# Kernel tuning notes

Hardware: AMD Instinct MI355X
Metric: run time of the kernel (lower is better)

The kernel has to match this reference:

```python
import jax, jax.numpy as jnp
import numpy as np
import math

VOCAB = 32000; D = 256; H = 8; HD = D // H; S = 2048; MLP = 1024; NC = 2
B = 4; L = 4; VEC = 8; M = S // VEC; MMA_K = 16; SPARSITY = 0.9


def _pos_encoding():
    pos = jnp.arange(S, dtype=jnp.float32)[:, None]
    div = jnp.exp(jnp.arange(0, D, 2, dtype=jnp.float32) * (-math.log(10000.0) / D))
    ang = pos * div  # [S, D//2]
    # interleave sin (even dims) / cos (odd dims)
    return jnp.stack([jnp.sin(ang), jnp.cos(ang)], axis=-1).reshape(S, D)


def _ln(x, g, b):
    mu = x.mean(-1, keepdims=True)
    var = x.var(-1, keepdims=True)
    return (x - mu) / jnp.sqrt(var + 1e-5) * g + b


def setup_inputs() -> dict:
    rng = np.random.default_rng(0)
    # nnz per block-row, aligned to mma_k_dim as in static_random_mask_aligned
    nnz = max(MMA_K, int(S * (1.0 - SPARSITY)) // MMA_K * MMA_K)
    mask = np.zeros((L, M, S), dtype=bool)
    for l in range(L):
        idx = np.argsort(rng.random((M, S)), axis=1)[:, :nnz]
        np.put_along_axis(mask[l], idx, True, axis=1)
    k = jax.random.key(0)
    ks = jax.random.split(k, 8)
    f = jnp.float32
    w = lambda key, shape, s=0.02: jax.random.normal(key, shape, dtype=f) * s
    return dict(
        x=jax.random.randint(ks[0], (B, S), 0, VOCAB),
        mask=jnp.asarray(mask),
        emb=w(ks[1], (VOCAB, D), 1.0),
        ln1_g=jnp.ones((L, D), f), ln1_b=jnp.zeros((L, D), f),
        in_w=w(ks[2], (L, 3 * D, D)), in_b=jnp.zeros((L, 3 * D), f),
        out_w=w(ks[3], (L, D, D)), out_b=jnp.zeros((L, D), f),
        ln2_g=jnp.ones((L, D), f), ln2_b=jnp.zeros((L, D), f),
        w1=w(ks[4], (L, MLP, D)), b1=jnp.zeros((L, MLP), f),
        w2=w(ks[5], (L, D, MLP)), b2=jnp.zeros((L, D), f),
        lnf_g=jnp.ones((D,), f), lnf_b=jnp.zeros((D,), f),
        wf=w(ks[6], (NC, D)), bf=jnp.zeros((NC,), f),
    )


def reference(x, mask, emb, ln1_g, ln1_b, in_w, in_b, out_w, out_b,
              ln2_g, ln2_b, w1, b1, w2, b2, lnf_g, lnf_b, wf, bf):
    h = emb[x] * jnp.sqrt(jnp.float32(D))          # [B,S,D]
    h = jnp.transpose(h, (1, 0, 2)) + _pos_encoding()[:, None, :]  # [S,B,D]
    neg = jnp.finfo(jnp.float32).min
    scale = 1.0 / jnp.sqrt(jnp.float32(HD))
    for l in range(L):
        # expand block-row mask: each of M rows covers VEC consecutive queries
        mfull = jnp.repeat(mask[l], VEC, axis=0)   # [S,S]
        o = _ln(h, ln1_g[l], ln1_b[l])
        qkv = o @ in_w[l].T + in_b[l]              # [S,B,3D]
        q, kk, v = [t.reshape(S, B, H, HD) for t in jnp.split(qkv, 3, axis=-1)]
        scores = jnp.einsum('sbhd,tbhd->bhst', q * scale, kk)
        scores = jnp.where(mfull[None, None], scores, neg)
        att = jax.nn.softmax(scores, axis=-1)
        ao = jnp.einsum('bhst,tbhd->sbhd', att, v).reshape(S, B, D)
        h2 = ao @ out_w[l].T + out_b[l] + h        # attn residual (block input)
        o2 = _ln(h2, ln2_g[l], ln2_b[l])
        ff = (o2 @ w1[l].T + b1[l]) @ w2[l].T + b2[l]  # note: no activation, per source
        h = ff + h                                  # final residual uses BLOCK INPUT, per source
    o = _ln(h, lnf_g, lnf_b)
    return o @ wf.T + bf                            # [S,B,NC]
```

## Files before the change

### kernel.cpp

```cpp
#include <hip/hip_runtime.h>
#include <hip/hip_bf16.h>
#include <math.h>

#define D_ 256
#define S_ 2048
#define B_ 4
#define H_ 8
#define HD_ 32
#define MLP_ 1024
#define L_ 4
#define M_ 256
#define NNZ 192
#define ROWS 8192

typedef __attribute__((ext_vector_type(8))) short bf16x8;
typedef __attribute__((ext_vector_type(8))) unsigned short u16x8;
typedef __attribute__((ext_vector_type(4))) float f32x4;
typedef __attribute__((ext_vector_type(4))) int i32x4;

__device__ __forceinline__ unsigned short f2bf(float f) {
    union { float f; unsigned u; } c; c.f = f;
    unsigned r = (c.u + 0x7FFFu + ((c.u >> 16) & 1u)) >> 16;
    return (unsigned short)r;
}
__device__ __forceinline__ float bf2f(unsigned short u) {
    union { unsigned u; float f; } c; c.u = (unsigned)u << 16;
    return c.f;
}

__global__ __launch_bounds__(256) void detect_mask_kernel(const unsigned int* __restrict__ mask,
                                                          int* __restrict__ flag) {
    int i = blockIdx.x * 256 + threadIdx.x;
    uint4 v = *(const uint4*)&mask[i * 4];
    bool hit = ((v.x | v.y | v.z | v.w) & 0x0000FF00u) != 0;
    if (__ballot(hit)) {
        if ((threadIdx.x & 63) == 0) atomicOr(flag, 1);
        else if (hit) atomicOr(flag, 1);
    }
}

__global__ __launch_bounds__(256) void build_idx_kernel(const void* __restrict__ mask,
                                                        int* __restrict__ idx,
                                                        const int* __restrict__ flagp) {
    int wave = threadIdx.x >> 6, lane = threadIdx.x & 63;
    int row = blockIdx.x * 4 + wave;
    int isbyte = *flagp;
    const unsigned char* mb = (const unsigned char*)mask;
    const int* mi = (const int*)mask;
    int base = 0;
    for (int c = 0; c < S_ / 64; c++) {
        int t = c * 64 + lane;
        size_t off = (size_t)row * S_ + t;
        bool bit = isbyte ? (mb[off] != 0) : (mi[off] != 0);
        unsigned long long bm = __ballot(bit);
        if (bit) {
            int pos = base + __popcll(bm & ((1ull << lane) - 1ull));
            if (pos < NNZ) idx[row * NNZ + pos] = t;
        }
        base += __popcll(bm);
    }
}

__global__ __launch_bounds__(256) void cvt_all_kernel(const float* __restrict__ in_w,
                                                      const float* __restrict__ out_w,
                                                      const float* __restrict__ w1,
                                                      const float* __restrict__ w2,
                                                      unsigned short* __restrict__ in_w_bf,
                                                      unsigned short* __restrict__ out_w_bf,
                                                      unsigned short* __restrict__ w1_bf,
                                                      unsigned short* __restrict__ w2_bf) {
    int i = blockIdx.x * 256 + threadIdx.x;
    const float* src; unsigned short* dst; int off;
    if (i < 196608)      { src = in_w;  dst = in_w_bf;  off = i; }
    else if (i < 262144) { src = out_w; dst = out_w_bf; off = i - 196608; }
    else if (i < 524288) { src = w1;    dst = w1_bf;    off = i - 262144; }
    else                 { src = w2;    dst = w2_bf;    off = i - 524288; }
    float4 v = *(const float4*)&src[(size_t)off * 4];
    ushort4 o;
    o.x = f2bf(v.x); o.y = f2bf(v.y); o.z = f2bf(v.z); o.w = f2bf(v.w);
    *(ushort4*)&dst[(size_t)off * 4] = o;
}

__global__ __launch_bounds__(256) void embed_kernel(const int* __restrict__ x,
                                                    const float* __restrict__ emb,
                                                    float* __restrict__ h) {
    int e = blockIdx.x * 256 + threadIdx.x;
    int r = e >> 7, i = e & 127;
    int s = r >> 2, b = r & 3;
    int tok = x[b * S_ + s];
    float div = expf(-(float)(2 * i) * (9.210340371976184f / 256.0f));
    float ang = (float)s * div;
    float sv = sinf(ang), cv = cosf(ang);
    float2 ev = *(const float2*)&emb[(size_t)tok * D_ + 2 * i];
    float2 hv;
    hv.x = ev.x * 16.0f + sv;
    hv.y = ev.y * 16.0f + cv;
    *(float2*)&h[(size_t)r * D_ + 2 * i] = hv;
}

__global__ __launch_bounds__(256) void ln_kernel(const float* __restrict__ x,
                                                 const float* __restrict__ g,
                                                 const float* __restrict__ b,
                                                 unsigned short* __restrict__ o) {
    int row = blockIdx.x * 4 + (threadIdx.x >> 6);
    int lane = threadIdx.x & 63;
    float4 v = *(const float4*)&x[(size_t)row * D_ + lane * 4];
    float s = v.x + v.y + v.z + v.w;
    float ss = v.x * v.x + v.y * v.y + v.z * v.z + v.w * v.w;
#pragma unroll
    for (int off = 32; off; off >>= 1) {
        s += __shfl_xor(s, off, 64);
        ss += __shfl_xor(ss, off, 64);
    }
    float mu = s * (1.0f / 256.0f);
    float var = ss * (1.0f / 256.0f) - mu * mu;
    float rstd = rsqrtf(var + 1e-5f);
    float4 gv = *(const float4*)&g[lane * 4];
    float4 bv = *(const float4*)&b[lane * 4];
    ushort4 ov;
    ov.x = f2bf((v.x - mu) * rstd * gv.x + bv.x);
    ov.y = f2bf((v.y - mu) * rstd * gv.y + bv.y);
    ov.z = f2bf((v.z - mu) * rstd * gv.z + bv.z);
    ov.w = f2bf((v.w - mu) * rstd * gv.w + bv.w);
    *(ushort4*)&o[(size_t)row * D_ + lane * 4] = ov;
}

#define BM 128
#define BN 64
#define BK 32
#define PK 40

template<int OUT_BF16>
__global__ __launch_bounds__(256) void gemm_bf16_nt(const unsigned short* __restrict__ A,
                                                    const unsigned short* __restrict__ W,
                                                    const float* __restrict__ bias,
                                                    const float* __restrict__ res,
                                                    void* __restrict__ Cp,
                                                    int N, int K) {
    __shared__ unsigned short As[BM * PK];
    __shared__ unsigned short Ws[BN * PK];
    int tid = threadIdx.x;
    int m0 = blockIdx.y * BM, n0 = blockIdx.x * BN;
    int w = tid >> 6, l = tid & 63;
    int wr = (w >> 1) * 64, wc = (w & 1) * 32;

    f32x4 acc[4][2];
#pragma unroll
    for (int mi = 0; mi < 4; mi++)
#pragma unroll
        for (int ni = 0; ni < 2; ni++) acc[mi][ni] = (f32x4){0.f, 0.f, 0.f, 0.f};

    int arow = tid >> 1, ak = (tid & 1) * 16;
    int wrow = tid >> 2, wk = (tid & 3) * 8;
    const unsigned short* Ag = &A[(size_t)(m0 + arow) * K + ak];
    const unsigned short* Wg = &W[(size_t)(n0 + wrow) * K + wk];

    int rl = l & 15, koff = (l >> 4) * 8;

    for (int kt = 0; kt < K; kt += BK) {
        i32x4 a0 = *(const i32x4*)(Ag + kt);
        i32x4 a1 = *(const i32x4*)(Ag + kt + 8);
        i32x4 w0 = *(const i32x4*)(Wg + kt);
        __syncthreads();
        *(i32x4*)&As[arow * PK + ak] = a0;
        *(i32x4*)&As[arow * PK + ak + 8] = a1;
        *(i32x4*)&Ws[wrow * PK + wk] = w0;
        __syncthreads();
        bf16x8 af[4], wf[2];
#pragma unroll
        for (int mi = 0; mi < 4; mi++)
            af[mi] = *(const bf16x8*)&As[(wr + mi * 16 + rl) * PK + koff];
#pragma unroll
        for (int ni = 0; ni < 2; ni++)
            wf[ni] = *(const bf16x8*)&Ws[(wc + ni * 16 + rl) * PK + koff];
#pragma unroll
        for (int mi = 0; mi < 4; mi++)
#pragma unroll
            for (int ni = 0; ni < 2; ni++)
                acc[mi][ni] = __builtin_amdgcn_mfma_f32_16x16x32_bf16(af[mi], wf[ni], acc[mi][ni], 0, 0, 0);
    }

    int col = l & 15, rbase = (l >> 4) * 4;
#pragma unroll
    for (int mi = 0; mi < 4; mi++) {
#pragma unroll
        for (int ni = 0; ni < 2; ni++) {
            int c = n0 + wc + ni * 16 + col;
            float bv = bias[c];
#pragma unroll
            for (int j = 0; j < 4; j++) {
                int r = m0 + wr + mi * 16 + rbase + j;
                float v = acc[mi][ni][j] + bv;
                if (res) v += res[(size_t)r * N + c];
                if (OUT_BF16) ((unsigned short*)Cp)[(size_t)r * N + c] = f2bf(v);
                else ((float*)Cp)[(size_t)r * N + c] = v;
            }
        }
    }
}

#define KSTR 40
#define VSTR 196
#define PSTR 200

__global__ __launch_bounds__(256, 3) void attn_kernel(const unsigned short* __restrict__ qkv,
                                                      const int* __restrict__ idx,
                                                      unsigned short* __restrict__ ao) {
    __shared__ int cols[NNZ];
    __shared__ float Qt[8][HD_];
    __shared__ unsigned short Kt[NNZ * KSTR];
    __shared__ float Vt[HD_ * VSTR];
    __shared__ float P[8 * PSTR];
    __shared__ float part[2][8][HD_];

    int blk = blockIdx.x;
    int m = blk & 255, hh = (blk >> 8) & 7, b = blk >> 11;
    int tid = threadIdx.x;
    if (tid < NNZ) cols[tid] = idx[m * NNZ + tid];
    {
        int q = tid >> 5, d = tid & 31;
        int s = m * 8 + q;
        Qt[q][d] = bf2f(qkv[((size_t)(s * B_ + b)) * 768 + hh * HD_ + d]) * 0.17677669529663687f;
    }
    __syncthreads();

#pragma unroll
    for (int k = 0; k < 3; k++) {
        int e = tid + 256 * k;
        int j = e % NNZ;
        int c = e / NNZ;
        size_t base = ((size_t)(cols[j] * 4 + b)) * 768 + hh * HD_ + c * 8;
        i32x4 kv = *(const i32x4*)&qkv[base + 256];
        int cswz = c ^ ((j >> 3) & 3);
        *(i32x4*)&Kt[j * KSTR + cswz * 8] = kv;
        i32x4 vraw = *(const i32x4*)&qkv[base + 512];
        u16x8 vv = *(const u16x8*)&vraw;
#pragma unroll
        for (int i2 = 0; i2 < 8; i2++) {
            int d = c * 8 + i2;
            Vt[d * VSTR + ((((j >> 2) ^ c) << 2) | (j & 3))] = bf2f((unsigned short)vv[i2]);
        }
    }
    __syncthreads();

    int gp = tid >> 6, ln = tid & 63;
    float qr0[HD_], qr1[HD_];
#pragma unroll
    for (int c4 = 0; c4 < 8; c4++) {
        float4 t0 = *(const float4*)&Qt[2 * gp][c4 * 4];
        qr0[c4 * 4 + 0] = t0.x; qr0[c4 * 4 + 1] = t0.y; qr0[c4 * 4 + 2] = t0.z; qr0[c4 * 4 + 3] = t0.w;
        float4 t1 = *(const float4*)&Qt[2 * gp + 1][c4 * 4];
        qr1[c4 * 4 + 0] = t1.x; qr1[c4 * 4 + 1] = t1.y; qr1[c4 * 4 + 2] = t1.z; qr1[c4 * 4 + 3] = t1.w;
    }
    float sc0[3], sc1[3];
#pragma unroll
    for (int k3 = 0; k3 < 3; k3++) {
        int j = ln + 64 * k3;
        int swz = (j >> 3) & 3;
        float a0 = 0.f, a1 = 0.f;
#pragma unroll
        for (int c = 0; c < 4; c++) {
            bf16x8 kv8 = *(const bf16x8*)&Kt[j * KSTR + (c ^ swz) * 8];
#pragma unroll
            for (int i2 = 0; i2 < 8; i2++) {
                float kf = bf2f((unsigned short)kv8[i2]);
                a0 = fmaf(kf, qr0[c * 8 + i2], a0);
                a1 = fmaf(kf, qr1[c * 8 + i2], a1);
            }
        }
        sc0[k3] = a0; sc1[k3] = a1;
    }
    float mx0 = fmaxf(fmaxf(sc0[0], sc0[1]), sc0[2]);
    float mx1 = fmaxf(fmaxf(sc1[0], sc1[1]), sc1[2]);
#pragma unroll
    for (int off = 32; off; off >>= 1) {
        mx0 = fmaxf(mx0, __shfl_xor(mx0, off, 64));
        mx1 = fmaxf(mx1, __shfl_xor(mx1, off, 64));
    }
    float e0[3], e1[3], s0 = 0.f, s1 = 0.f;
#pragma unroll
    for (int k3 = 0; k3 < 3; k3++) {
        e0[k3] = __expf(sc0[k3] - mx0); s0 += e0[k3];
        e1[k3] = __expf(sc1[k3] - mx1); s1 += e1[k3];
    }
#pragma unroll
    for (int off = 32; off; off >>= 1) {
        s0 += __shfl_xor(s0, off, 64);
        s1 += __shfl_xor(s1, off, 64);
    }
    float inv0 = 1.0f / s0, inv1 = 1.0f / s1;
#pragma unroll
    for (int k3 = 0; k3 < 3; k3++) {
        int j = ln + 64 * k3;
        P[(2 * gp) * PSTR + j] = e0[k3] * inv0;
        P[(2 * gp + 1) * PSTR + j] = e1[k3] * inv1;
    }
    __syncthreads();

    {
        int d = tid & 31;
        int pair = (tid >> 5) & 3;
        int jh = tid >> 7;
        int q0 = 2 * pair, q1 = q0 + 1;
        int sw = (d >> 3) & 3;
        float a0 = 0.f, a1 = 0.f;
#pragma unroll
        for (int gI = 0; gI < 24; gI++) {
            int jg = jh * 24 + gI;
            float4 vv = *(const float4*)&Vt[d * VSTR + ((jg ^ sw) << 2)];
            float4 p0 = *(const float4*)&P[q0 * PSTR + jg * 4];
            float4 p1 = *(const float4*)&P[q1 * PSTR + jg * 4];
            a0 += vv.x * p0.x + vv.y * p0.y + vv.z * p0.z + vv.w * p0.w;
            a1 += vv.x * p1.x + vv.y * p1.y + vv.z * p1.z + vv.w * p1.w;
        }
        part[jh][q0][d] = a0;
        part[jh][q1][d] = a1;
    }
    __syncthreads();
    {
        int q = tid >> 5, d = tid & 31;
        float r = part[0][q][d] + part[1][q][d];
        int s = m * 8 + q;
        ao[((size_t)(s * B_ + b)) * D_ + hh * HD_ + d] = f2bf(r);
    }
}

__global__ __launch_bounds__(256) void final_kernel(const float* __restrict__ h,
                                                    const float* __restrict__ g,
                                                    const float* __restrict__ b,
                                                    const float* __restrict__ wf,
                                                    const float* __restrict__ bf,
                                                    float* __restrict__ out) {
    int row = blockIdx.x * 4 + (threadIdx.x >> 6);
    int lane = threadIdx.x & 63;
    float4 v = *(const float4*)&h[(size_t)row * D_ + lane * 4];
    float s = v.x + v.y + v.z + v.w;
    float ss = v.x * v.x + v.y * v.y + v.z * v.z + v.w * v.w;
#pragma unroll
    for (int off = 32; off; off >>= 1) {
        s += __shfl_xor(s, off, 64);
        ss += __shfl_xor(ss, off, 64);
    }
    float mu = s * (1.0f / 256.0f);
    float var = ss * (1.0f / 256.0f) - mu * mu;
    float rstd = rsqrtf(var + 1e-5f);
    float4 gv = *(const float4*)&g[lane * 4];
    float4 bv = *(const float4*)&b[lane * 4];
    float o0 = (v.x - mu) * rstd * gv.x + bv.x;
    float o1 = (v.y - mu) * rstd * gv.y + bv.y;
    float o2 = (v.z - mu) * rstd * gv.z + bv.z;
    float o3 = (v.w - mu) * rstd * gv.w + bv.w;
    float4 w0 = *(const float4*)&wf[lane * 4];
    float4 w1 = *(const float4*)&wf[D_ + lane * 4];
    float a0 = o0 * w0.x + o1 * w0.y + o2 * w0.z + o3 * w0.w;
    float a1 = o0 * w1.x + o1 * w1.y + o2 * w1.z + o3 * w1.w;
#pragma unroll
    for (int off = 32; off; off >>= 1) {
        a0 += __shfl_xor(a0, off, 64);
        a1 += __shfl_xor(a1, off, 64);
    }
    if (lane == 0) {
        out[(size_t)row * 2 + 0] = a0 + bf[0];
        out[(size_t)row * 2 + 1] = a1 + bf[1];
    }
}

extern "C" void kernel_launch(void* const* d_in, const int* in_sizes, int n_in,
                              void* d_out, int out_size, void* d_ws, size_t ws_size,
                              hipStream_t stream) {
    const int* x = (const int*)d_in[0];
    const void* mask = d_in[1];
    const float* emb = (const float*)d_in[2];
    const float* ln1_g = (const float*)d_in[3];
    const float* ln1_b = (const float*)d_in[4];
    const float* in_w = (const float*)d_in[5];
    const float* in_b = (const float*)d_in[6];
    const float* out_w = (const float*)d_in[7];
    const float* out_b = (const float*)d_in[8];
    const float* ln2_g = (const float*)d_in[9];
    const float* ln2_b = (const float*)d_in[10];
    const float* w1 = (const float*)d_in[11];
    const float* b1 = (const float*)d_in[12];
    const float* w2 = (const float*)d_in[13];
    const float* b2 = (const float*)d_in[14];
    const float* lnf_g = (const float*)d_in[15];
    const float* lnf_b = (const float*)d_in[16];
    const float* wf = (const float*)d_in[17];
    const float* bfp = (const float*)d_in[18];
    float* out = (float*)d_out;

    const size_t MB = 1024 * 1024;
    char* ws = (char*)d_ws;
    int* idx = (int*)ws;
    int* flag = (int*)(ws + 786432);
    float* h = (float*)(ws + 1 * MB);
    unsigned short* o = (unsigned short*)(ws + 9 * MB);
    unsigned short* ao = o;
    float* h2 = (float*)(ws + 13 * MB);
    unsigned short* qkvb = (unsigned short*)(ws + 21 * MB);
    unsigned short* ff1 = (unsigned short*)(ws + 21 * MB);
    unsigned short* wbf = (unsigned short*)(ws + 37 * MB);
    unsigned short* in_w_bf = wbf;
    unsigned short* out_w_bf = wbf + 786432;
    unsigned short* w1_bf = wbf + 1048576;
    unsigned short* w2_bf = wbf + 2097152;

    hipMemsetAsync(flag, 0, sizeof(int), stream);
    detect_mask_kernel<<<16, 256, 0, stream>>>((const unsigned int*)mask, flag);
    build_idx_kernel<<<L_ * M_ / 4, 256, 0, stream>>>(mask, idx, flag);
    cvt_all_kernel<<<3072, 256, 0, stream>>>(in_w, out_w, w1, w2,
                                             in_w_bf, out_w_bf, w1_bf, w2_bf);
    embed_kernel<<<ROWS * (D_ / 2) / 256, 256, 0, stream>>>(x, emb, h);

    for (int l = 0; l < L_; l++) {
        ln_kernel<<<ROWS / 4, 256, 0, stream>>>(h, ln1_g + l * D_, ln1_b + l * D_, o);
        gemm_bf16_nt<1><<<dim3(768 / BN, ROWS / BM), 256, 0, stream>>>(
            o, in_w_bf + (size_t)l * 768 * D_, in_b + l * 768, nullptr, qkvb, 768, D_);
        attn_kernel<<<B_ * H_ * M_, 256, 0, stream>>>(qkvb, idx + l * M_ * NNZ, ao);
        gemm_bf16_nt<0><<<dim3(D_ / BN, ROWS / BM), 256, 0, stream>>>(
            ao, out_w_bf + (size_t)l * D_ * D_, out_b + l * D_, h, h2, D_, D_);
        ln_kernel<<<ROWS / 4, 256, 0, stream>>>(h2, ln2_g + l * D_, ln2_b + l * D_, o);
        gemm_bf16_nt<1><<<dim3(MLP_ / BN, ROWS / BM), 256, 0, stream>>>(
            o, w1_bf + (size_t)l * MLP_ * D_, b1 + l * MLP_, nullptr, ff1, MLP_, D_);
        gemm_bf16_nt<0><<<dim3(D_ / BN, ROWS / BM), 256, 0, stream>>>(
            ff1, w2_bf + (size_t)l * D_ * MLP_, b2 + l * D_, h, h, D_, MLP_);
    }
    final_kernel<<<ROWS / 4, 256, 0, stream>>>(h, lnf_g, lnf_b, wf, bfp, out);
}
```

Measured before the change: 721.2 us.

## Use bf16 MFMA for sparse attention QK and PV with bf16 LDS tiles

Rewrites the attention kernel to compute Q·K scores and P·V with 16x16x32 bf16 MFMA instructions instead of scalar FMA loops. K, V and probabilities are kept as bf16 in shared memory, which shrinks the LDS footprint and allows four blocks per CU instead of three. The softmax max and sum are combined across waves through small shared arrays. The 8 queries are padded to 16 MFMA rows, so half of each MFMA is wasted. Probabilities are rounded to bf16 and the K/V swizzles are dropped, which may cause LDS bank conflicts.

```diff
diff --git a/kernel.cpp b/kernel.cpp
--- a/kernel.cpp
+++ b/kernel.cpp
@@ -199,29 +199,27 @@
     }
 }
 
-#define KSTR 40
-#define VSTR 196
-#define PSTR 200
-
-__global__ __launch_bounds__(256, 3) void attn_kernel(const unsigned short* __restrict__ qkv,
+#define KST 40
+#define VST 200
+
+__global__ __launch_bounds__(256, 4) void attn_kernel(const unsigned short* __restrict__ qkv,
                                                       const int* __restrict__ idx,
                                                       unsigned short* __restrict__ ao) {
     __shared__ int cols[NNZ];
-    __shared__ float Qt[8][HD_];
-    __shared__ unsigned short Kt[NNZ * KSTR];
-    __shared__ float Vt[HD_ * VSTR];
-    __shared__ float P[8 * PSTR];
-    __shared__ float part[2][8][HD_];
+    __shared__ unsigned short Kt[NNZ * KST];
+    __shared__ unsigned short Vt[HD_ * VST];
+    __shared__ unsigned short Pl[8 * VST];
+    __shared__ float mpart[4][8];
+    __shared__ float spart[4][8];
 
     int blk = blockIdx.x;
     int m = blk & 255, hh = (blk >> 8) & 7, b = blk >> 11;
     int tid = threadIdx.x;
+    int w = tid >> 6;
+    int gg = (tid >> 4) & 3;
+    int rl = tid & 15;
+
     if (tid < NNZ) cols[tid] = idx[m * NNZ + tid];
-    {
-        int q = tid >> 5, d = tid & 31;
-        int s = m * 8 + q;
-        Qt[q][d] = bf2f(qkv[((size_t)(s * B_ + b)) * 768 + hh * HD_ + d]) * 0.17677669529663687f;
-    }
     __syncthreads();
 
 #pragma unroll
@@ -231,97 +229,94 @@
         int c = e / NNZ;
         size_t base = ((size_t)(cols[j] * 4 + b)) * 768 + hh * HD_ + c * 8;
         i32x4 kv = *(const i32x4*)&qkv[base + 256];
-        int cswz = c ^ ((j >> 3) & 3);
-        *(i32x4*)&Kt[j * KSTR + cswz * 8] = kv;
-        i32x4 vraw = *(const i32x4*)&qkv[base + 512];
-        u16x8 vv = *(const u16x8*)&vraw;
-#pragma unroll
-        for (int i2 = 0; i2 < 8; i2++) {
-            int d = c * 8 + i2;
-            Vt[d * VSTR + ((((j >> 2) ^ c) << 2) | (j & 3))] = bf2f((unsigned short)vv[i2]);
-        }
+        *(i32x4*)&Kt[j * KST + c * 8] = kv;
+        u16x8 vv = *(const u16x8*)&qkv[base + 512];
+#pragma unroll
+        for (int i2 = 0; i2 < 8; i2++)
+            Vt[(c * 8 + i2) * VST + j] = vv[i2];
+    }
+    bf16x8 afq;
+    if (rl < 8) {
+        size_t qa = ((size_t)((m * 8 + rl) * 4 + b)) * 768 + hh * HD_ + gg * 8;
+        afq = *(const bf16x8*)&qkv[qa];
+    } else {
+        afq = (bf16x8){0, 0, 0, 0, 0, 0, 0, 0};
     }
     __syncthreads();
 
-    int gp = tid >> 6, ln = tid & 63;
-    float qr0[HD_], qr1[HD_];
-#pragma unroll
-    for (int c4 = 0; c4 < 8; c4++) {
-        float4 t0 = *(const float4*)&Qt[2 * gp][c4 * 4];
-        qr0[c4 * 4 + 0] = t0.x; qr0[c4 * 4 + 1] = t0.y; qr0[c4 * 4 + 2] = t0.z; qr0[c4 * 4 + 3] = t0.w;
-        float4 t1 = *(const float4*)&Qt[2 * gp + 1][c4 * 4];
-        qr1[c4 * 4 + 0] = t1.x; qr1[c4 * 4 + 1] = t1.y; qr1[c4 * 4 + 2] = t1.z; qr1[c4 * 4 + 3] = t1.w;
-    }
-    float sc0[3], sc1[3];
-#pragma unroll
-    for (int k3 = 0; k3 < 3; k3++) {
-        int j = ln + 64 * k3;
-        int swz = (j >> 3) & 3;
-        float a0 = 0.f, a1 = 0.f;
-#pragma unroll
-        for (int c = 0; c < 4; c++) {
-            bf16x8 kv8 = *(const bf16x8*)&Kt[j * KSTR + (c ^ swz) * 8];
-#pragma unroll
-            for (int i2 = 0; i2 < 8; i2++) {
-                float kf = bf2f((unsigned short)kv8[i2]);
-                a0 = fmaf(kf, qr0[c * 8 + i2], a0);
-                a1 = fmaf(kf, qr1[c * 8 + i2], a1);
+    f32x4 acc[3];
+#pragma unroll
+    for (int t = 0; t < 3; t++) {
+        int jt = w * 3 + t;
+        bf16x8 bk = *(const bf16x8*)&Kt[(jt * 16 + rl) * KST + gg * 8];
+        acc[t] = __builtin_amdgcn_mfma_f32_16x16x32_bf16(afq, bk,
+                   (f32x4){0.f, 0.f, 0.f, 0.f}, 0, 0, 0);
+    }
+
+    float mv[4];
+#pragma unroll
+    for (int r = 0; r < 4; r++) {
+        float mx = fmaxf(fmaxf(acc[0][r], acc[1][r]), acc[2][r]);
+#pragma unroll
+        for (int off = 1; off <= 8; off <<= 1) mx = fmaxf(mx, __shfl_xor(mx, off, 64));
+        mv[r] = mx;
+    }
+    if (rl == 0 && gg < 2) {
+#pragma unroll
+        for (int r = 0; r < 4; r++) mpart[w][gg * 4 + r] = mv[r];
+    }
+    __syncthreads();
+    int qbase = (gg & 1) * 4;
+    float mx[4], ev[3][4], sv[4];
+#pragma unroll
+    for (int r = 0; r < 4; r++) {
+        float a = fmaxf(fmaxf(mpart[0][qbase + r], mpart[1][qbase + r]),
+                        fmaxf(mpart[2][qbase + r], mpart[3][qbase + r]));
+        mx[r] = a;
+        float s = 0.f;
+#pragma unroll
+        for (int t = 0; t < 3; t++) {
+            ev[t][r] = __expf((acc[t][r] - a) * 0.17677669529663687f);
+            s += ev[t][r];
+        }
+#pragma unroll
+        for (int off = 1; off <= 8; off <<= 1) s += __shfl_xor(s, off, 64);
+        sv[r] = s;
+    }
+    if (rl == 0 && gg < 2) {
+#pragma unroll
+        for (int r = 0; r < 4; r++) spart[w][gg * 4 + r] = sv[r];
+    }
+    __syncthreads();
+    if (gg < 2) {
+#pragma unroll
+        for (int r = 0; r < 4; r++) {
+            float inv = 1.0f / (spart[0][qbase + r] + spart[1][qbase + r] +
+                                spart[2][qbase + r] + spart[3][qbase + r]);
+            int q = gg * 4 + r;
+#pragma unroll
+            for (int t = 0; t < 3; t++)
+                Pl[q * VST + (w * 3 + t) * 16 + rl] = f2bf(ev[t][r] * inv);
+        }
+    }
+    __syncthreads();
+
+    if (w < 2) {
+        f32x4 oacc = (f32x4){0.f, 0.f, 0.f, 0.f};
+#pragma unroll
+        for (int ks = 0; ks < 6; ks++) {
+            bf16x8 ap = *(const bf16x8*)&Pl[(rl & 7) * VST + ks * 32 + gg * 8];
+            bf16x8 bv = *(const bf16x8*)&Vt[(w * 16 + rl) * VST + ks * 32 + gg * 8];
+            oacc = __builtin_amdgcn_mfma_f32_16x16x32_bf16(ap, bv, oacc, 0, 0, 0);
+        }
+        if (gg < 2) {
+#pragma unroll
+            for (int r = 0; r < 4; r++) {
+                int q = gg * 4 + r;
+                size_t oa = ((size_t)((m * 8 + q) * 4 + b)) * 256 + hh * HD_ + w * 16 + rl;
+                ao[oa] = f2bf(oacc[r]);
             }
         }
-        sc0[k3] = a0; sc1[k3] = a1;
-    }
-    float mx0 = fmaxf(fmaxf(sc0[0], sc0[1]), sc0[2]);
-    float mx1 = fmaxf(fmaxf(sc1[0], sc1[1]), sc1[2]);
-#pragma unroll
-    for (int off = 32; off; off >>= 1) {
-        mx0 = fmaxf(mx0, __shfl_xor(mx0, off, 64));
-        mx1 = fmaxf(mx1, __shfl_xor(mx1, off, 64));
-    }
-    float e0[3], e1[3], s0 = 0.f, s1 = 0.f;
-#pragma unroll
-    for (int k3 = 0; k3 < 3; k3++) {
-        e0[k3] = __expf(sc0[k3] - mx0); s0 += e0[k3];
-        e1[k3] = __expf(sc1[k3] - mx1); s1 += e1[k3];
-    }
-#pragma unroll
-    for (int off = 32; off; off >>= 1) {
-        s0 += __shfl_xor(s0, off, 64);
-        s1 += __shfl_xor(s1, off, 64);
-    }
-    float inv0 = 1.0f / s0, inv1 = 1.0f / s1;
-#pragma unroll
-    for (int k3 = 0; k3 < 3; k3++) {
-        int j = ln + 64 * k3;
-        P[(2 * gp) * PSTR + j] = e0[k3] * inv0;
-        P[(2 * gp + 1) * PSTR + j] = e1[k3] * inv1;
-    }
-    __syncthreads();
-
-    {
-        int d = tid & 31;
-        int pair = (tid >> 5) & 3;
-        int jh = tid >> 7;
-        int q0 = 2 * pair, q1 = q0 + 1;
-        int sw = (d >> 3) & 3;
-        float a0 = 0.f, a1 = 0.f;
-#pragma unroll
-        for (int gI = 0; gI < 24; gI++) {
-            int jg = jh * 24 + gI;
-            float4 vv = *(const float4*)&Vt[d * VSTR + ((jg ^ sw) << 2)];
-            float4 p0 = *(const float4*)&P[q0 * PSTR + jg * 4];
-            float4 p1 = *(const float4*)&P[q1 * PSTR + jg * 4];
-            a0 += vv.x * p0.x + vv.y * p0.y + vv.z * p0.z + vv.w * p0.w;
-            a1 += vv.x * p1.x + vv.y * p1.y + vv.z * p1.z + vv.w * p1.w;
-        }
-        part[jh][q0][d] = a0;
-        part[jh][q1][d] = a1;
-    }
-    __syncthreads();
-    {
-        int q = tid >> 5, d = tid & 31;
-        float r = part[0][q][d] + part[1][q][d];
-        int s = m * 8 + q;
-        ao[((size_t)(s * B_ + b)) * D_ + hh * HD_ + d] = f2bf(r);
     }
 }
 
```

New measurement: 650.6 us. -9.8%, faster.
